# Optimization experiments

Measured on AMD Instinct MI355X. Metric: run time of the kernel, lower is better.

The kernel has to match this reference:

```python
import jax, jax.numpy as jnp
import numpy as np

B, N, C, CS, CP, H, L = 1, 2048, 128, 128, 16, 4, 3
NQ, NK = 32, 128  # local attention window: n_queries, n_keys
EPS = 1e-5


def _make_beta(n):
    l = np.arange(n)[:, None]
    m = np.arange(n)[None, :]
    con = np.zeros((n, n), dtype=bool)
    for c in np.arange(NQ / 2, n, NQ):
        con |= (np.abs(l - c) < NQ / 2) & (np.abs(m - c) < NK / 2)
    return np.where(con, 0.0, -1e10).astype(np.float32)


def setup_inputs() -> dict:
    key = jax.random.key(0)
    ks = iter(jax.random.split(key, 32))
    w = lambda *shape: jax.random.normal(next(ks), shape, dtype=jnp.float32) * 0.02
    inp = {
        'a': jax.random.normal(next(ks), (B, N, C), dtype=jnp.float32),
        's': jax.random.normal(next(ks), (B, N, CS), dtype=jnp.float32),
        'z': jax.random.normal(next(ks), (B, N, N, CP), dtype=jnp.float32),
        'beta': jnp.asarray(_make_beta(N))[None],
        'ada1_ln_w': jnp.ones((L, CS)), 'ada1_lin_w': w(L, CS, C),
        'ada1_lin_b': jnp.zeros((L, C)), 'ada1_nb_w': w(L, CS, C),
        'lnz_w': jnp.ones((L, CP)), 'lnz_b': jnp.zeros((L, CP)),
        'zinj_w': w(L, CP, H),
        'q_w': w(L, C, C), 'q_b': jnp.zeros((L, C)),
        'k_w': w(L, C, C), 'v_w': w(L, C, C),
        'g_w': w(L, C, C), 'o_w': w(L, C, C),
        'agate_w': w(L, CS, C), 'agate_b': jnp.full((L, C), -2.0),
        'ada2_ln_w': jnp.ones((L, CS)), 'ada2_lin_w': w(L, CS, C),
        'ada2_lin_b': jnp.zeros((L, C)), 'ada2_nb_w': w(L, CS, C),
        'lin1_w': w(L, C, 2 * C), 'lin2_w': w(L, C, 2 * C), 'lin3_w': w(L, 2 * C, C),
        'tgate_w': w(L, CS, C), 'tgate_b': jnp.full((L, C), -2.0),
    }
    return inp


def _ln(x):
    mu = jnp.mean(x, axis=-1, keepdims=True)
    var = jnp.var(x, axis=-1, keepdims=True)
    return (x - mu) * jax.lax.rsqrt(var + EPS)


def _adaln(a, s, ln_w, lin_w, lin_b, nb_w):
    # AdaLN: LN(a) gated & shifted by LN(s)
    a = _ln(a)
    sn = _ln(s) * ln_w
    return jax.nn.sigmoid(sn @ lin_w + lin_b) * a + sn @ nb_w


def _forward(a, s, z, beta, ada1_ln_w, ada1_lin_w, ada1_lin_b, ada1_nb_w,
             lnz_w, lnz_b, zinj_w, q_w, q_b, k_w, v_w, g_w, o_w,
             agate_w, agate_b, ada2_ln_w, ada2_lin_w, ada2_lin_b, ada2_nb_w,
             lin1_w, lin2_w, lin3_w, tgate_w, tgate_b):
    b_, n_, c_ = a.shape
    h_ = zinj_w.shape[-1]
    d_ = c_ // h_
    scale = 1.0 / np.sqrt(d_).astype(np.float32)
    zn0 = _ln(z)  # shared pre-affine LN of pair rep
    for i in range(q_w.shape[0]):
        # --- AttentionPairBias ---
        ah = _adaln(a, s, ada1_ln_w[i], ada1_lin_w[i], ada1_lin_b[i], ada1_nb_w[i])
        zb = jnp.einsum('bijc,ch->bhij', zn0 * lnz_w[i] + lnz_b[i], zinj_w[i])
        q = ((ah @ q_w[i] + q_b[i]) * scale).reshape(b_, n_, h_, d_)
        k = (ah @ k_w[i]).reshape(b_, n_, h_, d_)
        v = (ah @ v_w[i]).reshape(b_, n_, h_, d_)
        scores = jnp.einsum('bihd,bjhd->bhij', q, k) + zb + beta[:, None]
        p = jax.nn.softmax(scores, axis=-1)
        o = jnp.einsum('bhij,bjhd->bihd', p, v).reshape(b_, n_, c_)
        o = o * jax.nn.sigmoid(ah @ g_w[i])
        attn = (o @ o_w[i]) * jax.nn.sigmoid(s @ agate_w[i] + agate_b[i])
        # --- ConditionedTransitionBlock ---
        th = _adaln(a, s, ada2_ln_w[i], ada2_lin_w[i], ada2_lin_b[i], ada2_nb_w[i])
        bb = jax.nn.silu(th @ lin1_w[i]) * (th @ lin2_w[i])
        trans = jax.nn.sigmoid(s @ tgate_w[i] + tgate_b[i]) * th * (bb @ lin3_w[i])
        a = attn + trans
    return a


def reference(a, s, z, beta, ada1_ln_w, ada1_lin_w, ada1_lin_b, ada1_nb_w,
              lnz_w, lnz_b, zinj_w, q_w, q_b, k_w, v_w, g_w, o_w,
              agate_w, agate_b, ada2_ln_w, ada2_lin_w, ada2_lin_b, ada2_nb_w,
              lin1_w, lin2_w, lin3_w, tgate_w, tgate_b):
    return _forward(a, s, z, beta, ada1_ln_w, ada1_lin_w, ada1_lin_b, ada1_nb_w,
                    lnz_w, lnz_b, zinj_w, q_w, q_b, k_w, v_w, g_w, o_w,
                    agate_w, agate_b, ada2_ln_w, ada2_lin_w, ada2_lin_b, ada2_nb_w,
                    lin1_w, lin2_w, lin3_w, tgate_w, tgate_b)
```

## Files before the change

kernel.cpp:

```cpp
#include <hip/hip_runtime.h>


#define NT 2048

__device__ __forceinline__ float sig_(float x) { return 1.0f / (1.0f + __expf(-x)); }

__device__ __forceinline__ float redsum32(float v) {
#pragma unroll
  for (int o = 16; o > 0; o >>= 1) v += __shfl_xor(v, o);
  return v;
}

__device__ __forceinline__ void mm4(const float* __restrict__ W, int ldw,
                                    const float* As_row, int K, int c0, float* acc) {
  const float* __restrict__ wp = W + c0;
  for (int k = 0; k < K; k += 4) {
    float4 a4 = *(const float4*)(As_row + k);
#pragma unroll
    for (int kk = 0; kk < 4; ++kk) {
      float a = ((const float*)&a4)[kk];
      float4 w0 = *(const float4*)(wp);
      acc[0] = fmaf(a, w0.x, acc[0]);
      acc[1] = fmaf(a, w0.y, acc[1]);
      acc[2] = fmaf(a, w0.z, acc[2]);
      acc[3] = fmaf(a, w0.w, acc[3]);
      wp += ldw;
    }
  }
}

__device__ __forceinline__ void mm4x2(const float* __restrict__ W1,
                                      const float* __restrict__ W2, int ldw,
                                      const float* As_row, int K, int c0,
                                      float* acc1, float* acc2) {
  const float* __restrict__ wp1 = W1 + c0;
  const float* __restrict__ wp2 = W2 + c0;
  for (int k = 0; k < K; k += 4) {
    float4 a4 = *(const float4*)(As_row + k);
#pragma unroll
    for (int kk = 0; kk < 4; ++kk) {
      float a = ((const float*)&a4)[kk];
      float4 w0 = *(const float4*)(wp1);
      float4 u0 = *(const float4*)(wp2);
      acc1[0] = fmaf(a, w0.x, acc1[0]);
      acc1[1] = fmaf(a, w0.y, acc1[1]);
      acc1[2] = fmaf(a, w0.z, acc1[2]);
      acc1[3] = fmaf(a, w0.w, acc1[3]);
      acc2[0] = fmaf(a, u0.x, acc2[0]);
      acc2[1] = fmaf(a, u0.y, acc2[1]);
      acc2[2] = fmaf(a, u0.z, acc2[2]);
      acc2[3] = fmaf(a, u0.w, acc2[3]);
      wp1 += ldw; wp2 += ldw;
    }
  }
}

__global__ __launch_bounds__(256) void k_ln_rows(const float* __restrict__ X,
                                                 float* __restrict__ Y) {
  int row  = blockIdx.x * 4 + (threadIdx.x >> 6);
  int lane = threadIdx.x & 63;
  const float* xr = X + (size_t)row * 128;
  float x0 = xr[lane], x1 = xr[lane + 64];
  float s = x0 + x1;
#pragma unroll
  for (int o = 32; o > 0; o >>= 1) s += __shfl_xor(s, o);
  float mu = s * (1.0f / 128.0f);
  float d0 = x0 - mu, d1 = x1 - mu;
  float v = d0 * d0 + d1 * d1;
#pragma unroll
  for (int o = 32; o > 0; o >>= 1) v += __shfl_xor(v, o);
  float rs = rsqrtf(v * (1.0f / 128.0f) + 1e-5f);
  float* yr = Y + (size_t)row * 128;
  yr[lane] = d0 * rs;
  yr[lane + 64] = d1 * rs;
}

__global__ __launch_bounds__(256) void k_gates(
    const float* __restrict__ s, const float* __restrict__ agw,
    const float* __restrict__ agb, const float* __restrict__ tgw,
    const float* __restrict__ tgb, float* __restrict__ gatesA,
    float* __restrict__ gatesT) {
  __shared__ float As[8 * 132];
  int r0 = blockIdx.x * 8;
  int bz = blockIdx.y;
  int l = bz % 3, which = bz / 3;
  const float* W = (which ? tgw : agw) + (size_t)l * 128 * 128;
  const float* bias = (which ? tgb : agb) + (size_t)l * 128;
  float* outp = (which ? gatesT : gatesA) + (size_t)l * NT * 128;
  int tid = threadIdx.x;
  int r = tid >> 5, sub = tid & 31;
  *(float4*)&As[r * 132 + sub * 4] =
      *(const float4*)(s + (size_t)(r0 + r) * 128 + sub * 4);
  __syncthreads();
  int c0 = sub << 2;
  float acc[4] = {0, 0, 0, 0};
  mm4(W, 128, &As[r * 132], 128, c0, acc);
  size_t base = (size_t)(r0 + r) * 128 + c0;
#pragma unroll
  for (int j = 0; j < 4; ++j) outp[base + j] = sig_(acc[j] + bias[c0 + j]);
}

__global__ __launch_bounds__(256) void k_adaln12(
    const float* __restrict__ a, const float* __restrict__ ln_s,
    const float* __restrict__ lnw1, const float* __restrict__ linw1,
    const float* __restrict__ linb1, const float* __restrict__ nbw1,
    const float* __restrict__ lnw2, const float* __restrict__ linw2,
    const float* __restrict__ linb2, const float* __restrict__ nbw2,
    float* __restrict__ ah, float* __restrict__ th) {
  __shared__ float Sn[8 * 132];
  __shared__ float La[8 * 132];
  int r0 = blockIdx.x * 8;
  int y = blockIdx.y;
  const float* lnw  = y ? lnw2 : lnw1;
  const float* linw = y ? linw2 : linw1;
  const float* linb = y ? linb2 : linb1;
  const float* nbw  = y ? nbw2 : nbw1;
  float* outp = y ? th : ah;
  int tid = threadIdx.x;
  int r = tid >> 5, sub = tid & 31;
  {
    float4 v = *(const float4*)(ln_s + (size_t)(r0 + r) * 128 + sub * 4);
    float4 sc = *(const float4*)(lnw + sub * 4);
    v.x *= sc.x; v.y *= sc.y; v.z *= sc.z; v.w *= sc.w;
    *(float4*)&Sn[r * 132 + sub * 4] = v;
  }
  {
    float4 x = *(const float4*)(a + (size_t)(r0 + r) * 128 + sub * 4);
    float s = redsum32(x.x + x.y + x.z + x.w);
    float mu = s * (1.0f / 128.0f);
    float4 d = make_float4(x.x - mu, x.y - mu, x.z - mu, x.w - mu);
    float v = redsum32(d.x * d.x + d.y * d.y + d.z * d.z + d.w * d.w);
    float rs = rsqrtf(v * (1.0f / 128.0f) + 1e-5f);
    d.x *= rs; d.y *= rs; d.z *= rs; d.w *= rs;
    *(float4*)&La[r * 132 + sub * 4] = d;
  }
  __syncthreads();
  int c0 = sub << 2;
  float acc1[4] = {0, 0, 0, 0}, acc2[4] = {0, 0, 0, 0};
  mm4x2(linw, nbw, 128, &Sn[r * 132], 128, c0, acc1, acc2);
  size_t base = (size_t)(r0 + r) * 128 + c0;
#pragma unroll
  for (int j = 0; j < 4; ++j) {
    float g = sig_(acc1[j] + linb[c0 + j]);
    outp[base + j] = g * La[r * 132 + c0 + j] + acc2[j];
  }
}

__global__ __launch_bounds__(256) void k_qkvg(
    const float* __restrict__ ah, const float* __restrict__ qw,
    const float* __restrict__ kw, const float* __restrict__ vw,
    const float* __restrict__ gw, const float* __restrict__ qb,
    float* __restrict__ qkvg) {
  __shared__ float As[8 * 132];
  int r0 = blockIdx.x * 8;
  int mat = blockIdx.y;
  const float* W = (mat == 0) ? qw : (mat == 1) ? kw : (mat == 2) ? vw : gw;
  int tid = threadIdx.x;
  int r = tid >> 5, sub = tid & 31;
  *(float4*)&As[r * 132 + sub * 4] =
      *(const float4*)(ah + (size_t)(r0 + r) * 128 + sub * 4);
  __syncthreads();
  int c0 = sub << 2;
  float acc[4] = {0, 0, 0, 0};
  mm4(W, 128, &As[r * 132], 128, c0, acc);
  float* op = qkvg + (size_t)(r0 + r) * 512 + mat * 128 + c0;
  if (mat == 0) {
#pragma unroll
    for (int j = 0; j < 4; ++j)
      op[j] = (acc[j] + qb[c0 + j]) * 0.17677669529663687f;
  } else if (mat == 3) {
#pragma unroll
    for (int j = 0; j < 4; ++j) op[j] = sig_(acc[j]);
  } else {
#pragma unroll
    for (int j = 0; j < 4; ++j) op[j] = acc[j];
  }
}

__global__ __launch_bounds__(256) void k_wattn(
    const float* __restrict__ qkvg, const float* __restrict__ z,
    const float* __restrict__ lnzw, const float* __restrict__ lnzb,
    const float* __restrict__ zinj, float* __restrict__ og,
    float* __restrict__ colpart) {
  __shared__ float Qs[8][128];
  __shared__ float S[8][4][132];
  __shared__ float KV[32][128];
  __shared__ float wz[4][16];
  __shared__ float bzw[2][4];
  __shared__ float red[2][128];

  const int tid = threadIdx.x;
  const int bx = blockIdx.x;
  if (bx >= 256) {
    int b = bx - 256;
    int rr = tid >> 7, c = tid & 127;
    float acc = 0.0f;
    for (int t = 0; t < 16; ++t) {
      int row = b * 32 + rr + t * 2;
      acc += qkvg[(size_t)row * 512 + 256 + c];
    }
    red[rr][c] = acc;
    __syncthreads();
    if (rr == 0) colpart[b * 128 + c] = red[0][c] + red[1][c];
    return;
  }

  const int win = bx >> 2, sub4 = bx & 3;
  const int cen = 16 + 32 * win;
  const int i0 = cen - 15 + 8 * sub4;
  const int nrows = (sub4 == 3) ? 7 : 8;
  const int jlo = max(0, cen - 63), jhi = min(2047, cen + 63);
  const int nk = jhi - jlo + 1;

  if (tid < 64) {
    int h = tid & 3, c = tid >> 2;
    wz[h][c] = lnzw[c] * zinj[c * 4 + h];
  }
  if (tid < 8) {
    int h = tid & 3, which = tid >> 2;
    float acc = 0.0f;
    for (int c = 0; c < 16; ++c) acc += (which ? lnzb[c] : lnzw[c]) * zinj[c * 4 + h];
    bzw[which][h] = acc;
  }
  {
    int r = tid >> 5, sub = tid & 31;
    int i = i0 + min(r, nrows - 1);
    *(float4*)&Qs[r][sub * 4] = *(const float4*)(qkvg + (size_t)i * 512 + sub * 4);
  }
  __syncthreads();

  for (int idx = tid; idx < 8 * 128; idx += 256) {
    int r = idx >> 7, jj = idx & 127;
    if (jj < nk) {
      int i = i0 + min(r, nrows - 1);
      int j = jlo + jj;
      const float* zp = z + ((size_t)i * 2048 + j) * 16;
      float x[16];
      *(float4*)&x[0]  = *(const float4*)(zp + 0);
      *(float4*)&x[4]  = *(const float4*)(zp + 4);
      *(float4*)&x[8]  = *(const float4*)(zp + 8);
      *(float4*)&x[12] = *(const float4*)(zp + 12);
      float sm = 0.0f;
#pragma unroll
      for (int c = 0; c < 16; ++c) sm += x[c];
      float mu = sm * (1.0f / 16.0f);
      float var = 0.0f;
#pragma unroll
      for (int c = 0; c < 16; ++c) { float d = x[c] - mu; var = fmaf(d, d, var); }
      float rs = rsqrtf(var * (1.0f / 16.0f) + 1e-5f);
#pragma unroll
      for (int h = 0; h < 4; ++h) {
        float dot = 0.0f;
#pragma unroll
        for (int c = 0; c < 16; ++c) dot = fmaf(x[c], wz[h][c], dot);
        S[r][h][jj] = fmaf(rs, dot - mu * bzw[0][h], bzw[1][h]);
      }
    } else {
#pragma unroll
      for (int h = 0; h < 4; ++h) S[r][h][jj] = -1e30f;
    }
  }
  __syncthreads();

  {
    const int r = tid >> 5, h = (tid >> 3) & 3, part = tid & 7;
    float qreg[32];
#pragma unroll
    for (int d4 = 0; d4 < 32; d4 += 4)
      *(float4*)&qreg[d4] = *(const float4*)&Qs[r][h * 32 + d4];
    for (int kb = 0; kb < 128; kb += 32) {
      for (int idx = tid; idx < 32 * 32; idx += 256) {
        int kk = idx >> 5, c4 = (idx & 31) << 2;
        int j = jlo + kb + kk;
        int cs = (c4 + ((kk >> 3) << 2)) & 127;
        float4 val = make_float4(0.f, 0.f, 0.f, 0.f);
        if (j <= jhi) val = *(const float4*)(qkvg + (size_t)j * 512 + 128 + c4);
        *(float4*)&KV[kk][cs] = val;
      }
      __syncthreads();
#pragma unroll
      for (int u = 0; u < 4; ++u) {
        int jj = part + (u << 3);
        int rot = (jj >> 3) << 2;
        float dot = 0.0f;
#pragma unroll
        for (int d4 = 0; d4 < 32; d4 += 4) {
          int cs = (h * 32 + d4 + rot) & 127;
          float4 kv = *(const float4*)&KV[jj][cs];
          dot = fmaf(qreg[d4 + 0], kv.x, dot);
          dot = fmaf(qreg[d4 + 1], kv.y, dot);
          dot = fmaf(qreg[d4 + 2], kv.z, dot);
          dot = fmaf(qreg[d4 + 3], kv.w, dot);
        }
        S[r][h][kb + jj] += dot;
      }
      __syncthreads();
    }
  }

  {
    const int rh = tid >> 3, part = tid & 7;
    const int sr = rh >> 2, sh = rh & 3;
    float* Srow = &S[sr][sh][0];
    float m = -1e30f;
#pragma unroll
    for (int st = 0; st < 16; ++st) m = fmaxf(m, Srow[part + (st << 3)]);
#pragma unroll
    for (int o = 4; o > 0; o >>= 1) m = fmaxf(m, __shfl_xor(m, o));
    float ss = 0.0f;
#pragma unroll
    for (int st = 0; st < 16; ++st) {
      int jj = part + (st << 3);
      float e = __expf(Srow[jj] - m);
      Srow[jj] = e;
      ss += e;
    }
#pragma unroll
    for (int o = 4; o > 0; o >>= 1) ss += __shfl_xor(ss, o);
    float inv = 1.0f / ss;
#pragma unroll
    for (int st = 0; st < 16; ++st) Srow[part + (st << 3)] *= inv;
  }
  __syncthreads();

  {
    const int r = tid >> 5, cg = tid & 31;
    const int ca = cg << 2;
    const int h = cg >> 3;
    float acc[4] = {0, 0, 0, 0};
    for (int kb = 0; kb < 128; kb += 32) {
      for (int idx = tid; idx < 32 * 32; idx += 256) {
        int kk = idx >> 5, c4 = (idx & 31) << 2;
        int j = jlo + kb + kk;
        int cs = (c4 + ((kk >> 3) << 2)) & 127;
        float4 val = make_float4(0.f, 0.f, 0.f, 0.f);
        if (j <= jhi) val = *(const float4*)(qkvg + (size_t)j * 512 + 256 + c4);
        *(float4*)&KV[kk][cs] = val;
      }
      __syncthreads();
#pragma unroll 4
      for (int kk = 0; kk < 32; ++kk) {
        int rot = (kk >> 3) << 2;
        float sa = S[r][h][kb + kk];
        float4 va = *(const float4*)&KV[kk][(ca + rot) & 127];
        acc[0] = fmaf(sa, va.x, acc[0]);
        acc[1] = fmaf(sa, va.y, acc[1]);
        acc[2] = fmaf(sa, va.z, acc[2]);
        acc[3] = fmaf(sa, va.w, acc[3]);
      }
      __syncthreads();
    }
    if (r < nrows) {
      int i = i0 + r;
      float4 ga = *(const float4*)(qkvg + (size_t)i * 512 + 384 + ca);
      float4 oa = make_float4(acc[0] * ga.x, acc[1] * ga.y, acc[2] * ga.z, acc[3] * ga.w);
      *(float4*)(og + (size_t)i * 128 + ca) = oa;
    }
  }
}

__global__ __launch_bounds__(256) void k_oproj(const float* __restrict__ og,
                                               const float* __restrict__ ow,
                                               const float* __restrict__ gA,
                                               const float* __restrict__ colpart,
                                               const float* __restrict__ qkvg,
                                               float* __restrict__ attn) {
  __shared__ float As[8 * 132];
  __shared__ float red[2][128];
  int r0 = blockIdx.x * 8;
  int tid = threadIdx.x;
  int r = tid >> 5, sub = tid & 31;
  *(float4*)&As[r * 132 + sub * 4] =
      *(const float4*)(og + (size_t)(r0 + r) * 128 + sub * 4);
  __syncthreads();
  if ((r0 & 31) == 0) {
    int col = tid & 127, half = tid >> 7;
    float acc = 0.0f;
    for (int b = half; b < 64; b += 2) acc += colpart[b * 128 + col];
    red[half][col] = acc;
    __syncthreads();
    if (half == 0) {
      float mv = (red[0][col] + red[1][col]) * (1.0f / 2048.0f);
      As[col] = mv * qkvg[(size_t)r0 * 512 + 384 + col];
    }
    __syncthreads();
  }
  int c0 = sub << 2;
  float acc[4] = {0, 0, 0, 0};
  mm4(ow, 128, &As[r * 132], 128, c0, acc);
  size_t base = (size_t)(r0 + r) * 128 + c0;
#pragma unroll
  for (int j = 0; j < 4; ++j) attn[base + j] = acc[j] * gA[base + j];
}

__global__ __launch_bounds__(256) void k_lin12(const float* __restrict__ th,
                                               const float* __restrict__ w1,
                                               const float* __restrict__ w2,
                                               float* __restrict__ bb) {
  __shared__ float As[8 * 132];
  int r0 = blockIdx.x * 8;
  int cb0 = blockIdx.y * 128;
  int tid = threadIdx.x;
  int r = tid >> 5, sub = tid & 31;
  *(float4*)&As[r * 132 + sub * 4] =
      *(const float4*)(th + (size_t)(r0 + r) * 128 + sub * 4);
  __syncthreads();
  int c0 = cb0 + (sub << 2);
  float acc1[4] = {0, 0, 0, 0}, acc2[4] = {0, 0, 0, 0};
  mm4x2(w1, w2, 256, &As[r * 132], 128, c0, acc1, acc2);
  size_t base = (size_t)(r0 + r) * 256 + c0;
#pragma unroll
  for (int j = 0; j < 4; ++j) {
    float x1 = acc1[j];
    bb[base + j] = x1 * sig_(x1) * acc2[j];
  }
}

__global__ __launch_bounds__(256) void k_lin3comb(
    const float* __restrict__ bb, const float* __restrict__ w3,
    const float* __restrict__ attn, const float* __restrict__ gT,
    const float* __restrict__ th, float* __restrict__ outp) {
  __shared__ float As[8 * 260];
  int r0 = blockIdx.x * 8;
  int tid = threadIdx.x;
  for (int idx = tid; idx < 8 * 64; idx += 256) {
    int row = idx >> 6, c4 = (idx & 63) << 2;
    *(float4*)&As[row * 260 + c4] = *(const float4*)(bb + (size_t)(r0 + row) * 256 + c4);
  }
  __syncthreads();
  int r = tid >> 5, sub = tid & 31;
  int c0 = sub << 2;
  float acc[4] = {0, 0, 0, 0};
  mm4(w3, 128, &As[r * 260], 256, c0, acc);
  size_t base = (size_t)(r0 + r) * 128 + c0;
#pragma unroll
  for (int j = 0; j < 4; ++j)
    outp[base + j] = attn[base + j] + gT[base + j] * th[base + j] * acc[j];
}

extern "C" void kernel_launch(void* const* d_in, const int* in_sizes, int n_in,
                              void* d_out, int out_size, void* d_ws, size_t ws_size,
                              hipStream_t stream) {
  (void)in_sizes; (void)n_in; (void)out_size; (void)ws_size;
  const float* A_in   = (const float*)d_in[0];
  const float* S_in   = (const float*)d_in[1];
  const float* Z_in   = (const float*)d_in[2];
  const float* ada1_ln_w  = (const float*)d_in[4];
  const float* ada1_lin_w = (const float*)d_in[5];
  const float* ada1_lin_b = (const float*)d_in[6];
  const float* ada1_nb_w  = (const float*)d_in[7];
  const float* lnz_w      = (const float*)d_in[8];
  const float* lnz_b      = (const float*)d_in[9];
  const float* zinj_w     = (const float*)d_in[10];
  const float* q_w        = (const float*)d_in[11];
  const float* q_b        = (const float*)d_in[12];
  const float* k_w        = (const float*)d_in[13];
  const float* v_w        = (const float*)d_in[14];
  const float* g_w        = (const float*)d_in[15];
  const float* o_w        = (const float*)d_in[16];
  const float* agate_w    = (const float*)d_in[17];
  const float* agate_b    = (const float*)d_in[18];
  const float* ada2_ln_w  = (const float*)d_in[19];
  const float* ada2_lin_w = (const float*)d_in[20];
  const float* ada2_lin_b = (const float*)d_in[21];
  const float* ada2_nb_w  = (const float*)d_in[22];
  const float* lin1_w     = (const float*)d_in[23];
  const float* lin2_w     = (const float*)d_in[24];
  const float* lin3_w     = (const float*)d_in[25];
  const float* tgate_w    = (const float*)d_in[26];
  const float* tgate_b    = (const float*)d_in[27];

  const int N = NT, C = 128;
  float* ws = (float*)d_ws;
  float* ln_s    = ws;
  float* ah      = ln_s + (size_t)N * C;
  float* th      = ah + (size_t)N * C;
  float* qkvg    = th + (size_t)N * C;
  float* og      = qkvg + (size_t)N * 512;
  float* attn    = og + (size_t)N * C;
  float* bb      = attn + (size_t)N * C;
  float* gatesA  = bb + (size_t)N * 256;
  float* gatesT  = gatesA + (size_t)3 * N * C;
  float* colpart = gatesT + (size_t)3 * N * C;

  dim3 blk(256);
  k_ln_rows<<<512, blk, 0, stream>>>(S_in, ln_s);
  k_gates<<<dim3(256, 6), blk, 0, stream>>>(S_in, agate_w, agate_b, tgate_w,
                                            tgate_b, gatesA, gatesT);
  const float* acur = A_in;
  for (int l = 0; l < 3; ++l) {
    k_adaln12<<<dim3(256, 2), blk, 0, stream>>>(
        acur, ln_s, ada1_ln_w + (size_t)l * C, ada1_lin_w + (size_t)l * C * C,
        ada1_lin_b + (size_t)l * C, ada1_nb_w + (size_t)l * C * C,
        ada2_ln_w + (size_t)l * C, ada2_lin_w + (size_t)l * C * C,
        ada2_lin_b + (size_t)l * C, ada2_nb_w + (size_t)l * C * C, ah, th);
    k_qkvg<<<dim3(256, 4), blk, 0, stream>>>(ah, q_w + (size_t)l * C * C,
                                             k_w + (size_t)l * C * C,
                                             v_w + (size_t)l * C * C,
                                             g_w + (size_t)l * C * C,
                                             q_b + (size_t)l * C, qkvg);
    k_lin12<<<dim3(256, 2), blk, 0, stream>>>(th, lin1_w + (size_t)l * C * 2 * C,
                                              lin2_w + (size_t)l * C * 2 * C, bb);
    k_wattn<<<320, blk, 0, stream>>>(qkvg, Z_in, lnz_w + (size_t)l * 16,
                                     lnz_b + (size_t)l * 16,
                                     zinj_w + (size_t)l * 64, og, colpart);
    k_oproj<<<256, blk, 0, stream>>>(og, o_w + (size_t)l * C * C,
                                     gatesA + (size_t)l * N * C, colpart, qkvg,
                                     attn);
    k_lin3comb<<<256, blk, 0, stream>>>(bb, lin3_w + (size_t)l * 2 * C * C, attn,
                                        gatesT + (size_t)l * N * C, th,
                                        (float*)d_out);
    acur = (const float*)d_out;
  }
}
```

Before: 780.6 us.

## Fuse kernels: inline s-LN into AdaLN, merge QKVG with lin12, fuse oproj and lin3

Drops the separate LayerNorm-of-s kernel and recomputes LN(s) inside the AdaLN kernel. Merges the QKVG projection with the lin1/lin2 SwiGLU projection into one 6-way launch, and fuses the output projection with lin3 and the final combine into a single 512-thread tail kernel. The aim is fewer launches and no attn round trip through memory. In exchange, LN(s) is recomputed on every layer, and the tail kernel gives each thread two columns, which means narrower weight loads.

```diff
diff --git a/kernel.cpp b/kernel.cpp
--- a/kernel.cpp
+++ b/kernel.cpp
@@ -55,24 +55,20 @@
   }
 }
 
-__global__ __launch_bounds__(256) void k_ln_rows(const float* __restrict__ X,
-                                                 float* __restrict__ Y) {
-  int row  = blockIdx.x * 4 + (threadIdx.x >> 6);
-  int lane = threadIdx.x & 63;
-  const float* xr = X + (size_t)row * 128;
-  float x0 = xr[lane], x1 = xr[lane + 64];
-  float s = x0 + x1;
-#pragma unroll
-  for (int o = 32; o > 0; o >>= 1) s += __shfl_xor(s, o);
-  float mu = s * (1.0f / 128.0f);
-  float d0 = x0 - mu, d1 = x1 - mu;
-  float v = d0 * d0 + d1 * d1;
-#pragma unroll
-  for (int o = 32; o > 0; o >>= 1) v += __shfl_xor(v, o);
-  float rs = rsqrtf(v * (1.0f / 128.0f) + 1e-5f);
-  float* yr = Y + (size_t)row * 128;
-  yr[lane] = d0 * rs;
-  yr[lane + 64] = d1 * rs;
+__device__ __forceinline__ void mm2(const float* __restrict__ W, int ldw,
+                                    const float* As_row, int K, int c0, float* acc) {
+  const float* __restrict__ wp = W + c0;
+  for (int k = 0; k < K; k += 4) {
+    float4 a4 = *(const float4*)(As_row + k);
+#pragma unroll
+    for (int kk = 0; kk < 4; ++kk) {
+      float a = ((const float*)&a4)[kk];
+      float2 w0 = *(const float2*)(wp);
+      acc[0] = fmaf(a, w0.x, acc[0]);
+      acc[1] = fmaf(a, w0.y, acc[1]);
+      wp += ldw;
+    }
+  }
 }
 
 __global__ __launch_bounds__(256) void k_gates(
@@ -101,7 +97,7 @@
 }
 
 __global__ __launch_bounds__(256) void k_adaln12(
-    const float* __restrict__ a, const float* __restrict__ ln_s,
+    const float* __restrict__ a, const float* __restrict__ s_in,
     const float* __restrict__ lnw1, const float* __restrict__ linw1,
     const float* __restrict__ linb1, const float* __restrict__ nbw1,
     const float* __restrict__ lnw2, const float* __restrict__ linw2,
@@ -119,15 +115,20 @@
   int tid = threadIdx.x;
   int r = tid >> 5, sub = tid & 31;
   {
-    float4 v = *(const float4*)(ln_s + (size_t)(r0 + r) * 128 + sub * 4);
+    float4 x = *(const float4*)(s_in + (size_t)(r0 + r) * 128 + sub * 4);
+    float sm = redsum32(x.x + x.y + x.z + x.w);
+    float mu = sm * (1.0f / 128.0f);
+    float4 d = make_float4(x.x - mu, x.y - mu, x.z - mu, x.w - mu);
+    float v = redsum32(d.x * d.x + d.y * d.y + d.z * d.z + d.w * d.w);
+    float rs = rsqrtf(v * (1.0f / 128.0f) + 1e-5f);
     float4 sc = *(const float4*)(lnw + sub * 4);
-    v.x *= sc.x; v.y *= sc.y; v.z *= sc.z; v.w *= sc.w;
-    *(float4*)&Sn[r * 132 + sub * 4] = v;
+    d.x *= rs * sc.x; d.y *= rs * sc.y; d.z *= rs * sc.z; d.w *= rs * sc.w;
+    *(float4*)&Sn[r * 132 + sub * 4] = d;
   }
   {
     float4 x = *(const float4*)(a + (size_t)(r0 + r) * 128 + sub * 4);
-    float s = redsum32(x.x + x.y + x.z + x.w);
-    float mu = s * (1.0f / 128.0f);
+    float sm = redsum32(x.x + x.y + x.z + x.w);
+    float mu = sm * (1.0f / 128.0f);
     float4 d = make_float4(x.x - mu, x.y - mu, x.z - mu, x.w - mu);
     float v = redsum32(d.x * d.x + d.y * d.y + d.z * d.z + d.w * d.w);
     float rs = rsqrtf(v * (1.0f / 128.0f) + 1e-5f);
@@ -146,34 +147,50 @@
   }
 }
 
-__global__ __launch_bounds__(256) void k_qkvg(
-    const float* __restrict__ ah, const float* __restrict__ qw,
-    const float* __restrict__ kw, const float* __restrict__ vw,
-    const float* __restrict__ gw, const float* __restrict__ qb,
-    float* __restrict__ qkvg) {
+__global__ __launch_bounds__(256) void k_proj6(
+    const float* __restrict__ ah, const float* __restrict__ th,
+    const float* __restrict__ qw, const float* __restrict__ kw,
+    const float* __restrict__ vw, const float* __restrict__ gw,
+    const float* __restrict__ qb, const float* __restrict__ w1,
+    const float* __restrict__ w2, float* __restrict__ qkvg,
+    float* __restrict__ bb) {
   __shared__ float As[8 * 132];
   int r0 = blockIdx.x * 8;
-  int mat = blockIdx.y;
-  const float* W = (mat == 0) ? qw : (mat == 1) ? kw : (mat == 2) ? vw : gw;
+  int y = blockIdx.y;
   int tid = threadIdx.x;
   int r = tid >> 5, sub = tid & 31;
+  const float* src = (y < 4) ? ah : th;
   *(float4*)&As[r * 132 + sub * 4] =
-      *(const float4*)(ah + (size_t)(r0 + r) * 128 + sub * 4);
-  __syncthreads();
-  int c0 = sub << 2;
-  float acc[4] = {0, 0, 0, 0};
-  mm4(W, 128, &As[r * 132], 128, c0, acc);
-  float* op = qkvg + (size_t)(r0 + r) * 512 + mat * 128 + c0;
-  if (mat == 0) {
-#pragma unroll
-    for (int j = 0; j < 4; ++j)
-      op[j] = (acc[j] + qb[c0 + j]) * 0.17677669529663687f;
-  } else if (mat == 3) {
-#pragma unroll
-    for (int j = 0; j < 4; ++j) op[j] = sig_(acc[j]);
+      *(const float4*)(src + (size_t)(r0 + r) * 128 + sub * 4);
+  __syncthreads();
+  if (y < 4) {
+    const float* W = (y == 0) ? qw : (y == 1) ? kw : (y == 2) ? vw : gw;
+    int c0 = sub << 2;
+    float acc[4] = {0, 0, 0, 0};
+    mm4(W, 128, &As[r * 132], 128, c0, acc);
+    float* op = qkvg + (size_t)(r0 + r) * 512 + y * 128 + c0;
+    if (y == 0) {
+#pragma unroll
+      for (int j = 0; j < 4; ++j)
+        op[j] = (acc[j] + qb[c0 + j]) * 0.17677669529663687f;
+    } else if (y == 3) {
+#pragma unroll
+      for (int j = 0; j < 4; ++j) op[j] = sig_(acc[j]);
+    } else {
+#pragma unroll
+      for (int j = 0; j < 4; ++j) op[j] = acc[j];
+    }
   } else {
-#pragma unroll
-    for (int j = 0; j < 4; ++j) op[j] = acc[j];
+    int cb0 = (y - 4) * 128;
+    int c0 = cb0 + (sub << 2);
+    float acc1[4] = {0, 0, 0, 0}, acc2[4] = {0, 0, 0, 0};
+    mm4x2(w1, w2, 256, &As[r * 132], 128, c0, acc1, acc2);
+    size_t base = (size_t)(r0 + r) * 256 + c0;
+#pragma unroll
+    for (int j = 0; j < 4; ++j) {
+      float x1 = acc1[j];
+      bb[base + j] = x1 * sig_(x1) * acc2[j];
+    }
   }
 }
 
@@ -359,83 +376,52 @@
   }
 }
 
-__global__ __launch_bounds__(256) void k_oproj(const float* __restrict__ og,
-                                               const float* __restrict__ ow,
-                                               const float* __restrict__ gA,
-                                               const float* __restrict__ colpart,
-                                               const float* __restrict__ qkvg,
-                                               float* __restrict__ attn) {
-  __shared__ float As[8 * 132];
+__global__ __launch_bounds__(512) void k_tail(
+    const float* __restrict__ og, const float* __restrict__ ow,
+    const float* __restrict__ gA, const float* __restrict__ colpart,
+    const float* __restrict__ qkvg, const float* __restrict__ bbuf,
+    const float* __restrict__ w3, const float* __restrict__ gT,
+    const float* __restrict__ th, float* __restrict__ outp) {
+  __shared__ float Ao[8 * 132];
+  __shared__ float Bb[8 * 260];
   __shared__ float red[2][128];
   int r0 = blockIdx.x * 8;
   int tid = threadIdx.x;
-  int r = tid >> 5, sub = tid & 31;
-  *(float4*)&As[r * 132 + sub * 4] =
-      *(const float4*)(og + (size_t)(r0 + r) * 128 + sub * 4);
+  int r = tid >> 6, sub = tid & 63;
+  if (sub < 32) {
+    *(float4*)&Ao[r * 132 + sub * 4] =
+        *(const float4*)(og + (size_t)(r0 + r) * 128 + sub * 4);
+  }
+  {
+    *(float4*)&Bb[r * 260 + sub * 4] =
+        *(const float4*)(bbuf + (size_t)(r0 + r) * 256 + sub * 4);
+  }
   __syncthreads();
   if ((r0 & 31) == 0) {
-    int col = tid & 127, half = tid >> 7;
-    float acc = 0.0f;
-    for (int b = half; b < 64; b += 2) acc += colpart[b * 128 + col];
-    red[half][col] = acc;
+    if (tid < 256) {
+      int col = tid & 127, half = tid >> 7;
+      float acc = 0.0f;
+      for (int b = half; b < 64; b += 2) acc += colpart[b * 128 + col];
+      red[half][col] = acc;
+    }
     __syncthreads();
-    if (half == 0) {
-      float mv = (red[0][col] + red[1][col]) * (1.0f / 2048.0f);
-      As[col] = mv * qkvg[(size_t)r0 * 512 + 384 + col];
+    if (tid < 128) {
+      float mv = (red[0][tid] + red[1][tid]) * (1.0f / 2048.0f);
+      Ao[tid] = mv * qkvg[(size_t)r0 * 512 + 384 + tid];
     }
     __syncthreads();
   }
-  int c0 = sub << 2;
-  float acc[4] = {0, 0, 0, 0};
-  mm4(ow, 128, &As[r * 132], 128, c0, acc);
+  int c0 = sub << 1;
+  float acc1[2] = {0, 0};
+  mm2(ow, 128, &Ao[r * 132], 128, c0, acc1);
+  float acc3[2] = {0, 0};
+  mm2(w3, 128, &Bb[r * 260], 256, c0, acc3);
   size_t base = (size_t)(r0 + r) * 128 + c0;
 #pragma unroll
-  for (int j = 0; j < 4; ++j) attn[base + j] = acc[j] * gA[base + j];
-}
-
-__global__ __launch_bounds__(256) void k_lin12(const float* __restrict__ th,
-                                               const float* __restrict__ w1,
-                                               const float* __restrict__ w2,
-                                               float* __restrict__ bb) {
-  __shared__ float As[8 * 132];
-  int r0 = blockIdx.x * 8;
-  int cb0 = blockIdx.y * 128;
-  int tid = threadIdx.x;
-  int r = tid >> 5, sub = tid & 31;
-  *(float4*)&As[r * 132 + sub * 4] =
-      *(const float4*)(th + (size_t)(r0 + r) * 128 + sub * 4);
-  __syncthreads();
-  int c0 = cb0 + (sub << 2);
-  float acc1[4] = {0, 0, 0, 0}, acc2[4] = {0, 0, 0, 0};
-  mm4x2(w1, w2, 256, &As[r * 132], 128, c0, acc1, acc2);
-  size_t base = (size_t)(r0 + r) * 256 + c0;
-#pragma unroll
-  for (int j = 0; j < 4; ++j) {
-    float x1 = acc1[j];
-    bb[base + j] = x1 * sig_(x1) * acc2[j];
-  }
-}
-
-__global__ __launch_bounds__(256) void k_lin3comb(
-    const float* __restrict__ bb, const float* __restrict__ w3,
-    const float* __restrict__ attn, const float* __restrict__ gT,
-    const float* __restrict__ th, float* __restrict__ outp) {
-  __shared__ float As[8 * 260];
-  int r0 = blockIdx.x * 8;
-  int tid = threadIdx.x;
-  for (int idx = tid; idx < 8 * 64; idx += 256) {
-    int row = idx >> 6, c4 = (idx & 63) << 2;
-    *(float4*)&As[row * 260 + c4] = *(const float4*)(bb + (size_t)(r0 + row) * 256 + c4);
-  }
-  __syncthreads();
-  int r = tid >> 5, sub = tid & 31;
-  int c0 = sub << 2;
-  float acc[4] = {0, 0, 0, 0};
-  mm4(w3, 128, &As[r * 260], 256, c0, acc);
-  size_t base = (size_t)(r0 + r) * 128 + c0;
-#pragma unroll
-  for (int j = 0; j < 4; ++j)
-    outp[base + j] = attn[base + j] + gT[base + j] * th[base + j] * acc[j];
+  for (int j = 0; j < 2; ++j) {
+    float attnv = acc1[j] * gA[base + j];
+    outp[base + j] = attnv + gT[base + j] * th[base + j] * acc3[j];
+  }
 }
 
 extern "C" void kernel_launch(void* const* d_in, const int* in_sizes, int n_in,
@@ -472,44 +458,37 @@
 
   const int N = NT, C = 128;
   float* ws = (float*)d_ws;
-  float* ln_s    = ws;
-  float* ah      = ln_s + (size_t)N * C;
+  float* ah      = ws;
   float* th      = ah + (size_t)N * C;
   float* qkvg    = th + (size_t)N * C;
   float* og      = qkvg + (size_t)N * 512;
-  float* attn    = og + (size_t)N * C;
-  float* bb      = attn + (size_t)N * C;
+  float* bb      = og + (size_t)N * C;
   float* gatesA  = bb + (size_t)N * 256;
   float* gatesT  = gatesA + (size_t)3 * N * C;
   float* colpart = gatesT + (size_t)3 * N * C;
 
   dim3 blk(256);
-  k_ln_rows<<<512, blk, 0, stream>>>(S_in, ln_s);
   k_gates<<<dim3(256, 6), blk, 0, stream>>>(S_in, agate_w, agate_b, tgate_w,
                                             tgate_b, gatesA, gatesT);
   const float* acur = A_in;
   for (int l = 0; l < 3; ++l) {
     k_adaln12<<<dim3(256, 2), blk, 0, stream>>>(
-        acur, ln_s, ada1_ln_w + (size_t)l * C, ada1_lin_w + (size_t)l * C * C,
+        acur, S_in, ada1_ln_w + (size_t)l * C, ada1_lin_w + (size_t)l * C * C,
         ada1_lin_b + (size_t)l * C, ada1_nb_w + (size_t)l * C * C,
         ada2_ln_w + (size_t)l * C, ada2_lin_w + (size_t)l * C * C,
         ada2_lin_b + (size_t)l * C, ada2_nb_w + (size_t)l * C * C, ah, th);
-    k_qkvg<<<dim3(256, 4), blk, 0, stream>>>(ah, q_w + (size_t)l * C * C,
-                                             k_w + (size_t)l * C * C,
-                                             v_w + (size_t)l * C * C,
-                                             g_w + (size_t)l * C * C,
-                                             q_b + (size_t)l * C, qkvg);
-    k_lin12<<<dim3(256, 2), blk, 0, stream>>>(th, lin1_w + (size_t)l * C * 2 * C,
-                                              lin2_w + (size_t)l * C * 2 * C, bb);
+    k_proj6<<<dim3(256, 6), blk, 0, stream>>>(
+        ah, th, q_w + (size_t)l * C * C, k_w + (size_t)l * C * C,
+        v_w + (size_t)l * C * C, g_w + (size_t)l * C * C, q_b + (size_t)l * C,
+        lin1_w + (size_t)l * C * 2 * C, lin2_w + (size_t)l * C * 2 * C, qkvg, bb);
     k_wattn<<<320, blk, 0, stream>>>(qkvg, Z_in, lnz_w + (size_t)l * 16,
                                      lnz_b + (size_t)l * 16,
                                      zinj_w + (size_t)l * 64, og, colpart);
-    k_oproj<<<256, blk, 0, stream>>>(og, o_w + (size_t)l * C * C,
-                                     gatesA + (size_t)l * N * C, colpart, qkvg,
-                                     attn);
-    k_lin3comb<<<256, blk, 0, stream>>>(bb, lin3_w + (size_t)l * 2 * C * C, attn,
-                                        gatesT + (size_t)l * N * C, th,
-                                        (float*)d_out);
+    k_tail<<<256, dim3(512), 0, stream>>>(og, o_w + (size_t)l * C * C,
+                                          gatesA + (size_t)l * N * C, colpart,
+                                          qkvg, bb, lin3_w + (size_t)l * 2 * C * C,
+                                          gatesT + (size_t)l * N * C, th,
+                                          (float*)d_out);
     acur = (const float*)d_out;
   }
 }
```

New measurement: 730.5 us. -6.4%, faster.
